# Performance work log

Hardware: AMD Instinct MI355X
Metric: run time of the kernel (lower is better)

The kernel has to match this reference:

```python
import jax, jax.numpy as jnp
import numpy as np

# pywt db4 decomposition filters (dec_lo, dec_hi), length 8
DB4_DEC_LO = np.array([-0.010597401784997278, 0.032883011666982945,
                       0.030841381835986965, -0.18703481171888114,
                       -0.02798376941698385, 0.6308807679295904,
                       0.7148465705525415, 0.23037781330885523], dtype=np.float32)
DB4_DEC_HI = np.array([-0.23037781330885523, 0.7148465705525415,
                       -0.6308807679295904, -0.02798376941698385,
                       0.18703481171888114, 0.030841381835986965,
                       -0.032883011666982945, -0.010597401784997278], dtype=np.float32)
LEVEL = 3


def setup_inputs() -> dict:
    key = jax.random.key(0)
    x = jax.random.normal(key, (64, 32, 4096), dtype=jnp.float32)  # (B, N, T)
    return {"x": x,
            "dec_lo": jnp.asarray(DB4_DEC_LO),
            "dec_hi": jnp.asarray(DB4_DEC_HI)}


def _swt(x, dec_lo, dec_hi, level=LEVEL):
    """Stationary (a trous) wavelet transform, matching ptwt.swt semantics."""
    B, N, T = x.shape
    filt_len = dec_lo.shape[0]
    # ptwt flips the filters so conv1d (correlation) performs true convolution
    filt = jnp.stack([dec_lo[::-1], dec_hi[::-1]], axis=0)[:, None, :]  # (2, 1, L)
    res_lo = x.reshape(B * N, 1, T)
    details = []
    for lvl in range(level):
        dil = 2 ** lvl
        padl = dil * (filt_len // 2 - 1)
        padr = dil * (filt_len // 2)
        padded = jnp.pad(res_lo, ((0, 0), (0, 0), (padl, padr)), mode="wrap")  # circular
        res = jax.lax.conv_general_dilated(
            padded, filt, window_strides=(1,), padding="VALID",
            rhs_dilation=(dil,), dimension_numbers=("NCH", "OIH", "NCH"))  # (BN, 2, T)
        res_lo = res[:, 0:1, :]
        details.append(res[:, 1, :])
    # ptwt ordering: [cA_level, cD_level, ..., cD_1]
    coeffs = [res_lo[:, 0, :]] + details[::-1]
    stacked = jnp.stack(coeffs, axis=1)  # (B*N, level+1, T)
    return stacked.reshape(B, N, level + 1, T).transpose(0, 1, 3, 2)  # (B, N, T, level+1)


def reference(x, dec_lo, dec_hi):
    return _swt(x, dec_lo, dec_hi)
```

## Files before the change

### kernel.cpp

```cpp
#include <hip/hip_runtime.h>

#define TLEN 4096
#define NTHREADS 256
#define PER (TLEN / NTHREADS)

__global__ __launch_bounds__(NTHREADS) void swt_db4_l3_kernel(
    const float* __restrict__ x,
    const float* __restrict__ lo_g,
    const float* __restrict__ hi_g,
    float* __restrict__ out)
{
    __shared__ float bufA[TLEN];
    __shared__ float bufB[TLEN];

    const int row = blockIdx.x;
    const int tid = threadIdx.x;

    float lo[8], hi[8];
#pragma unroll
    for (int j = 0; j < 8; ++j) { lo[j] = lo_g[j]; hi[j] = hi_g[j]; }

    const float* xr = x + (size_t)row * TLEN;

#pragma unroll
    for (int k = 0; k < PER / 4; ++k) {
        int idx = (tid + k * NTHREADS) * 4;
        float4 v = *reinterpret_cast<const float4*>(xr + idx);
        bufA[idx + 0] = v.x; bufA[idx + 1] = v.y;
        bufA[idx + 2] = v.z; bufA[idx + 3] = v.w;
    }
    __syncthreads();

    float D1[PER], D2[PER], D3[PER], A3[PER];

#pragma unroll
    for (int k = 0; k < PER; ++k) {
        int t = tid + k * NTHREADS;
        float a = 0.f, d = 0.f;
#pragma unroll
        for (int j = 0; j < 8; ++j) {
            float v = bufA[(t + (4 - j)) & (TLEN - 1)];
            a = fmaf(lo[j], v, a);
            d = fmaf(hi[j], v, d);
        }
        D1[k] = d;
        bufB[t] = a;
    }
    __syncthreads();

#pragma unroll
    for (int k = 0; k < PER; ++k) {
        int t = tid + k * NTHREADS;
        float a = 0.f, d = 0.f;
#pragma unroll
        for (int j = 0; j < 8; ++j) {
            float v = bufB[(t + (4 - j) * 2) & (TLEN - 1)];
            a = fmaf(lo[j], v, a);
            d = fmaf(hi[j], v, d);
        }
        D2[k] = d;
        bufA[t] = a;
    }
    __syncthreads();

#pragma unroll
    for (int k = 0; k < PER; ++k) {
        int t = tid + k * NTHREADS;
        float a = 0.f, d = 0.f;
#pragma unroll
        for (int j = 0; j < 8; ++j) {
            float v = bufA[(t + (4 - j) * 4) & (TLEN - 1)];
            a = fmaf(lo[j], v, a);
            d = fmaf(hi[j], v, d);
        }
        D3[k] = d;
        A3[k] = a;
    }

    float4* outr = reinterpret_cast<float4*>(out + (size_t)row * TLEN * 4);
#pragma unroll
    for (int k = 0; k < PER; ++k) {
        int t = tid + k * NTHREADS;
        outr[t] = make_float4(A3[k], D3[k], D2[k], D1[k]);
    }
}

extern "C" void kernel_launch(void* const* d_in, const int* in_sizes, int n_in,
                              void* d_out, int out_size, void* d_ws, size_t ws_size,
                              hipStream_t stream) {
    const float* x  = (const float*)d_in[0];
    const float* lo = (const float*)d_in[1];
    const float* hi = (const float*)d_in[2];
    float* out = (float*)d_out;

    const int rows = 64 * 32;
    swt_db4_l3_kernel<<<dim3(rows), dim3(NTHREADS), 0, stream>>>(x, lo, hi, out);
}
```

Baseline: 33.89 us.

## Double block size, add interior fast path, vector LDS stores, nontemporal output

Raises the threads per block from 256 to 512, which halves the per-thread register arrays. Adds a branch so interior samples use direct LDS addressing without the wraparound mask. Writes the input into LDS with one vector store instead of four scalar ones. Stores the output with nontemporal hints to avoid polluting the cache. The branch may diverge for threads near the edges, and the larger block size changes occupancy.

```diff
diff --git a/kernel.cpp b/kernel.cpp
--- a/kernel.cpp
+++ b/kernel.cpp
@@ -1,8 +1,33 @@
 #include <hip/hip_runtime.h>
 
 #define TLEN 4096
-#define NTHREADS 256
+#define NTHREADS 512
 #define PER (TLEN / NTHREADS)
+
+typedef float f32x4 __attribute__((ext_vector_type(4)));
+
+template<int DIL>
+__device__ __forceinline__ void swt_taps(const float* __restrict__ src, int t,
+                                         const float lo[8], const float hi[8],
+                                         float& a, float& d)
+{
+    a = 0.f; d = 0.f;
+    if (t >= 3 * DIL && t < TLEN - 4 * DIL) {
+#pragma unroll
+        for (int j = 0; j < 8; ++j) {
+            float v = src[t + (4 - j) * DIL];
+            a = fmaf(lo[j], v, a);
+            d = fmaf(hi[j], v, d);
+        }
+    } else {
+#pragma unroll
+        for (int j = 0; j < 8; ++j) {
+            float v = src[(t + (4 - j) * DIL) & (TLEN - 1)];
+            a = fmaf(lo[j], v, a);
+            d = fmaf(hi[j], v, d);
+        }
+    }
+}
 
 __global__ __launch_bounds__(NTHREADS) void swt_db4_l3_kernel(
     const float* __restrict__ x,
@@ -25,9 +50,8 @@
 #pragma unroll
     for (int k = 0; k < PER / 4; ++k) {
         int idx = (tid + k * NTHREADS) * 4;
-        float4 v = *reinterpret_cast<const float4*>(xr + idx);
-        bufA[idx + 0] = v.x; bufA[idx + 1] = v.y;
-        bufA[idx + 2] = v.z; bufA[idx + 3] = v.w;
+        f32x4 v = *reinterpret_cast<const f32x4*>(xr + idx);
+        *reinterpret_cast<f32x4*>(&bufA[idx]) = v;
     }
     __syncthreads();
 
@@ -36,13 +60,8 @@
 #pragma unroll
     for (int k = 0; k < PER; ++k) {
         int t = tid + k * NTHREADS;
-        float a = 0.f, d = 0.f;
-#pragma unroll
-        for (int j = 0; j < 8; ++j) {
-            float v = bufA[(t + (4 - j)) & (TLEN - 1)];
-            a = fmaf(lo[j], v, a);
-            d = fmaf(hi[j], v, d);
-        }
+        float a, d;
+        swt_taps<1>(bufA, t, lo, hi, a, d);
         D1[k] = d;
         bufB[t] = a;
     }
@@ -51,13 +70,8 @@
 #pragma unroll
     for (int k = 0; k < PER; ++k) {
         int t = tid + k * NTHREADS;
-        float a = 0.f, d = 0.f;
-#pragma unroll
-        for (int j = 0; j < 8; ++j) {
-            float v = bufB[(t + (4 - j) * 2) & (TLEN - 1)];
-            a = fmaf(lo[j], v, a);
-            d = fmaf(hi[j], v, d);
-        }
+        float a, d;
+        swt_taps<2>(bufB, t, lo, hi, a, d);
         D2[k] = d;
         bufA[t] = a;
     }
@@ -66,22 +80,19 @@
 #pragma unroll
     for (int k = 0; k < PER; ++k) {
         int t = tid + k * NTHREADS;
-        float a = 0.f, d = 0.f;
-#pragma unroll
-        for (int j = 0; j < 8; ++j) {
-            float v = bufA[(t + (4 - j) * 4) & (TLEN - 1)];
-            a = fmaf(lo[j], v, a);
-            d = fmaf(hi[j], v, d);
-        }
+        float a, d;
+        swt_taps<4>(bufA, t, lo, hi, a, d);
         D3[k] = d;
         A3[k] = a;
     }
 
-    float4* outr = reinterpret_cast<float4*>(out + (size_t)row * TLEN * 4);
+    f32x4* outr = reinterpret_cast<f32x4*>(out + (size_t)row * TLEN * 4);
 #pragma unroll
     for (int k = 0; k < PER; ++k) {
         int t = tid + k * NTHREADS;
-        outr[t] = make_float4(A3[k], D3[k], D2[k], D1[k]);
+        f32x4 v;
+        v.x = A3[k]; v.y = D3[k]; v.z = D2[k]; v.w = D1[k];
+        __builtin_nontemporal_store(v, &outr[t]);
     }
 }
 
```

Measured after the change: 42.97 us. 26.8% more time.
